# Optimization experiments

Hardware: AMD Instinct MI355X
Metric: run time of the kernel (lower is better)

Reference implementation:

```python
import jax, jax.numpy as jnp
import numpy as np

SIGMAS = (2.5, 4.0, 6.0, 9.0, 14.0)
TRUNCATE = 4.0
POOL = 16
COND_HIDDEN = 32


def _gauss_kernel_bank():
    """All K Gaussian kernels zero-padded (center-aligned) to a common length.
    Zero padding a centered symmetric kernel does not change the conv result,
    so a single grouped conv computes all K depthwise smoothings at once.
    Returns kernel bank [K, 1, L] and the common half-width pad."""
    ks = []
    for s in SIGMAS:
        r = max(1, int(TRUNCATE * s))
        xs = np.arange(-r, r + 1, dtype=np.float32)
        k = np.exp(-0.5 * (xs / s) ** 2)
        k = k / (k.sum() + 1e-12)
        ks.append(k)
    L = max(len(k) for k in ks)  # 113 for default sigmas
    bank = np.zeros((len(ks), 1, L), np.float32)
    for i, k in enumerate(ks):
        off = (L - len(k)) // 2
        bank[i, 0, off:off + len(k)] = k
    return jnp.asarray(bank), (L - 1) // 2


def setup_inputs() -> dict:
    key = jax.random.key(0)
    k0, k1, k2 = jax.random.split(key, 3)
    B, T, C = 16, 4096, 256
    H, K = COND_HIDDEN, len(SIGMAS)
    return {
        "x": jax.random.normal(k0, (B, T, C), jnp.float32),
        "W1": jax.random.normal(k1, (3, H), jnp.float32) * 0.5,
        "b1": jnp.zeros((H,), jnp.float32),
        "W2": jax.random.normal(k2, (H, K), jnp.float32) * 0.2,
        "b2": jnp.zeros((K,), jnp.float32),
    }


def reference(x, W1, b1, W2, b2):
    B, T, C = x.shape
    bank, pad = _gauss_kernel_bank()  # [K,1,L]
    # K depthwise Gaussian convs, fused into one grouped conv by treating
    # each (batch, channel) pair as an independent conv batch element.
    xin = x.transpose(0, 2, 1).reshape(B * C, 1, T)  # [B*C,1,T]
    y = jax.lax.conv_general_dilated(xin, bank, (1,), [(pad, pad)])  # [B*C,K,T]
    Y = y.reshape(B, C, -1, T).transpose(0, 3, 1, 2)  # [B,T,C,K]

    # local mean / variance with reflect padding (matches F.pad mode='reflect')
    pL = (POOL - 1) // 2
    pR = POOL - 1 - pL
    xp = jnp.pad(x, ((0, 0), (pL, pR), (0, 0)), mode="reflect")  # [B,T+POOL-1,C]
    cs = jnp.cumsum(xp, axis=1)
    cs = jnp.concatenate([jnp.zeros_like(cs[:, :1]), cs], axis=1)
    mean = (cs[:, POOL:] - cs[:, :-POOL]) / POOL  # [B,T,C]
    cs2 = jnp.cumsum(xp * xp, axis=1)
    cs2 = jnp.concatenate([jnp.zeros_like(cs2[:, :1]), cs2], axis=1)
    mean2 = (cs2[:, POOL:] - cs2[:, :-POOL]) / POOL
    var = jnp.maximum(mean2 - mean * mean, 0.0)

    # tiny per-position conditioner MLP -> softmax mixture weights over K
    feats = jnp.stack([mean, var, x], axis=-1)  # [B,T,C,3]
    h = jax.nn.gelu(feats @ W1 + b1, approximate=False)  # torch GELU = exact erf
    logits = h @ W2 + b2  # [B,T,C,K]
    w = jax.nn.softmax(logits, axis=-1)
    return (Y * w).sum(axis=-1)  # [B,T,C]
```

## Files before the change

### kernel.cpp

```cpp
#include <hip/hip_runtime.h>
#include <math.h>

#define T_LEN 4096
#define C_LEN 256
#define B_LEN 16

constexpr double cexp(double x) {
    double y = x * (1.0 / 1024.0);
    double t = 1.0, term = 1.0;
    for (int i = 1; i <= 12; ++i) { term *= y / i; t += term; }
    for (int i = 0; i < 10; ++i) t = t * t;
    return t;
}

constexpr int RAD[5] = {10, 16, 24, 36, 56};

struct Bank { float g[5][57]; };

constexpr Bank make_bank() {
    Bank b{};
    const double sig[5] = {2.5, 4.0, 6.0, 9.0, 14.0};
    for (int k = 0; k < 5; ++k) {
        double w[57] = {};
        for (int j = 0; j <= RAD[k]; ++j)
            w[j] = cexp(-0.5 * (double)(j * j) / (sig[k] * sig[k]));
        double s = w[0];
        for (int j = 1; j <= RAD[k]; ++j) s += 2.0 * w[j];
        s += 1e-12;
        for (int j = 0; j <= RAD[k]; ++j) b.g[k][j] = (float)(w[j] / s);
    }
    return b;
}

constexpr Bank BANK = make_bank();

#define LOG2E 1.4426950408889634f

__device__ __forceinline__ float fast_exp2(float x) {
#if __has_builtin(__builtin_amdgcn_exp2f)
    return __builtin_amdgcn_exp2f(x);
#else
    return __expf(x * 0.6931471805599453f);
#endif
}

__device__ __forceinline__ float gelu_fast(float v) {
    const float c1 = (float)(-2.0 * 0.7978845608028654 * 1.4426950408889634);
    const float c2 = c1 * 0.044715f;
    float v2 = v * v;
    float t  = fmaf(c2, v2, c1);
    float z  = v * t;
    float e  = fast_exp2(z);
    float r  = __builtin_amdgcn_rcpf(1.0f + e);
    return v * r;
}

__device__ __forceinline__ float ldz(const float* __restrict__ xb, int tt) {
    if (tt < 0 || tt >= T_LEN) return 0.0f;
    return xb[tt * C_LEN];
}

template <bool CHECKED>
__device__ __forceinline__ void work(const float* __restrict__ x,
                                     float* __restrict__ out,
                                     const float (*__restrict__ wle)[8],
                                     const float* __restrict__ w2e,
                                     const float* __restrict__ b2l,
                                     int b, int t0, int c) {
    const float* xb = x + (size_t)b * T_LEN * C_LEN + c;

    float v[19];
#pragma unroll
    for (int i = 0; i < 19; ++i) {
        int tt = t0 - 7 + i;
        if (CHECKED) {
            tt = (tt < 0) ? -tt : tt;
            tt = (tt >= T_LEN) ? (2 * T_LEN - 2 - tt) : tt;
        }
        v[i] = xb[tt * C_LEN];
    }

    float mean[4], var[4], xc[4];
    {
        float s = 0.f, q = 0.f;
#pragma unroll
        for (int i = 0; i < 16; ++i) { s += v[i]; q = fmaf(v[i], v[i], q); }
#pragma unroll
        for (int m = 0; m < 4; ++m) {
            if (m > 0) {
                float nw = v[15 + m], od = v[m - 1];
                s = s + nw - od;
                q = fmaf(nw, nw, fmaf(od, -od, q));
            }
            mean[m] = s * 0.0625f;
            float m2 = q * 0.0625f;
            float vv = fmaf(-mean[m], mean[m], m2);
            var[m] = vv > 0.f ? vv : 0.f;
            xc[m]  = v[7 + m];
        }
    }

    float acc[5][4];
#pragma unroll
    for (int k = 0; k < 5; ++k)
#pragma unroll
        for (int m = 0; m < 4; ++m) acc[k][m] = BANK.g[k][0] * xc[m];

    float F[4], Bw[4];
    if (CHECKED) {
        F[1] = ldz(xb, t0 + 1); F[2] = ldz(xb, t0 + 2);
        F[3] = ldz(xb, t0 + 3); F[0] = ldz(xb, t0 + 4);
        Bw[3] = ldz(xb, t0 - 1); Bw[0] = ldz(xb, t0);
        Bw[1] = ldz(xb, t0 + 1); Bw[2] = ldz(xb, t0 + 2);
    } else {
        F[1] = v[8]; F[2] = v[9]; F[3] = v[10]; F[0] = v[11];
        Bw[3] = v[6]; Bw[0] = v[7]; Bw[1] = v[8]; Bw[2] = v[9];
    }

#pragma unroll
    for (int j = 1; j <= 56; ++j) {
        float sm[4];
#pragma unroll
        for (int m = 0; m < 4; ++m)
            sm[m] = F[(j + m) & 3] + Bw[(m - j) & 3];
#pragma unroll
        for (int k = 0; k < 5; ++k) {
            if (j <= RAD[k]) {
#pragma unroll
                for (int m = 0; m < 4; ++m)
                    acc[k][m] = fmaf(BANK.g[k][j], sm[m], acc[k][m]);
            }
        }
        if (j < 56) {
            if (CHECKED) {
                F[j & 3]        = ldz(xb, t0 + j + 4);
                Bw[(3 - j) & 3] = ldz(xb, t0 - j - 1);
            } else {
                F[j & 3]        = (j <= 7) ? v[j + 11] : xb[(t0 + j + 4) * C_LEN];
                Bw[(3 - j) & 3] = (j <= 6) ? v[6 - j]  : xb[(t0 - j - 1) * C_LEN];
            }
        }
    }

    float lg[5][4];
#pragma unroll
    for (int k = 0; k < 5; ++k) {
        float bk = b2l[k];
#pragma unroll
        for (int m = 0; m < 4; ++m) lg[k][m] = bk;
    }

#pragma unroll 2
    for (int i = 0; i < 32; ++i) {
        float4 wa = *(const float4*)&wle[i][0];
        float4 wb = *(const float4*)&wle[i][4];
        float w24 = w2e[i];
#pragma unroll
        for (int m = 0; m < 4; ++m) {
            float pre = fmaf(wa.x, mean[m], fmaf(wa.y, var[m], fmaf(wa.z, xc[m], wa.w)));
            float h = gelu_fast(pre);
            lg[0][m] = fmaf(h, wb.x, lg[0][m]);
            lg[1][m] = fmaf(h, wb.y, lg[1][m]);
            lg[2][m] = fmaf(h, wb.z, lg[2][m]);
            lg[3][m] = fmaf(h, wb.w, lg[3][m]);
            lg[4][m] = fmaf(h, w24 , lg[4][m]);
        }
    }

#pragma unroll
    for (int m = 0; m < 4; ++m) {
        float l0 = lg[0][m], l1 = lg[1][m], l2 = lg[2][m], l3 = lg[3][m], l4 = lg[4][m];
        float mx = fmaxf(fmaxf(fmaxf(l0, l1), fmaxf(l2, l3)), l4);
        float e0 = fast_exp2(l0 - mx), e1 = fast_exp2(l1 - mx), e2 = fast_exp2(l2 - mx);
        float e3 = fast_exp2(l3 - mx), e4 = fast_exp2(l4 - mx);
        float den = ((e0 + e1) + (e2 + e3)) + e4;
        float num = e0 * acc[0][m];
        num = fmaf(e1, acc[1][m], num);
        num = fmaf(e2, acc[2][m], num);
        num = fmaf(e3, acc[3][m], num);
        num = fmaf(e4, acc[4][m], num);
        out[((size_t)b * T_LEN + t0 + m) * C_LEN + c] = num * __builtin_amdgcn_rcpf(den);
    }
}

__global__ __launch_bounds__(256) void agt_fused(
    const float* __restrict__ x, const float* __restrict__ W1,
    const float* __restrict__ b1, const float* __restrict__ W2,
    const float* __restrict__ b2, float* __restrict__ out) {
    __shared__ __align__(16) float wle[32][8];
    __shared__ float w2e[32];
    __shared__ float b2l[5];
    {
        int tid = threadIdx.x;
        if (tid < 32) {
            wle[tid][0] = W1[tid];
            wle[tid][1] = W1[32 + tid];
            wle[tid][2] = W1[64 + tid];
            wle[tid][3] = b1[tid];
            wle[tid][4] = W2[tid * 5 + 0] * LOG2E;
            wle[tid][5] = W2[tid * 5 + 1] * LOG2E;
            wle[tid][6] = W2[tid * 5 + 2] * LOG2E;
            wle[tid][7] = W2[tid * 5 + 3] * LOG2E;
            w2e[tid]    = W2[tid * 5 + 4] * LOG2E;
            if (tid < 5) b2l[tid] = b2[tid] * LOG2E;
        }
        __syncthreads();
    }
    int b     = blockIdx.x >> 10;
    int chunk = blockIdx.x & 1023;
    int t0    = chunk * 4;
    if (chunk >= 14 && chunk < 1010)
        work<false>(x, out, wle, w2e, b2l, b, t0, threadIdx.x);
    else
        work<true>(x, out, wle, w2e, b2l, b, t0, threadIdx.x);
}

extern "C" void kernel_launch(void* const* d_in, const int* in_sizes, int n_in,
                              void* d_out, int out_size, void* d_ws, size_t ws_size,
                              hipStream_t stream) {
    const float* x  = (const float*)d_in[0];
    const float* W1 = (const float*)d_in[1];
    const float* b1 = (const float*)d_in[2];
    const float* W2 = (const float*)d_in[3];
    const float* b2 = (const float*)d_in[4];
    float* out = (float*)d_out;

    (void)in_sizes; (void)n_in; (void)d_ws; (void)ws_size; (void)out_size;

    agt_fused<<<dim3(B_LEN * 1024), dim3(256), 0, stream>>>(x, W1, b1, W2, b2, out);
}
```

Before: 428.5 us.

## Run conditioner MLP on MFMA f16 matrix cores via per-wave LDS staging

Moves the per-position 3->32->5 conditioner MLP from scalar FMAs to MFMA 16x16x32 f16 instructions. Features (mean, var, x, 1) are packed to half precision in LDS, the hidden GELU activations are staged back through LDS as f16, and the logits are stored as f16 for the softmax. The goal is to cut the large VALU cost of the MLP, at the cost of f16 rounding of features, hidden values and logits. The softmax also drops the max subtraction, which risks overflow, and a min-blocks launch bound is added. Cross-lane LDS exchange relies only on compiler fences within a wave.

After: 1.263 ms. +194.7%, slower.

```diff
diff --git a/kernel.cpp b/kernel.cpp
--- a/kernel.cpp
+++ b/kernel.cpp
@@ -4,6 +4,8 @@
 #define T_LEN 4096
 #define C_LEN 256
 #define B_LEN 16
+#define LOG2E 1.4426950408889634f
+#define HSTR 80
 
 constexpr double cexp(double x) {
     double y = x * (1.0 / 1024.0);
@@ -34,7 +36,12 @@
 
 constexpr Bank BANK = make_bank();
 
-#define LOG2E 1.4426950408889634f
+typedef _Float16 hf;
+typedef hf    hfx2 __attribute__((ext_vector_type(2)));
+typedef hf    hfx8 __attribute__((ext_vector_type(8)));
+typedef float f32x4 __attribute__((ext_vector_type(4)));
+
+__device__ __forceinline__ void lds_fence() { asm volatile("" ::: "memory"); }
 
 __device__ __forceinline__ float fast_exp2(float x) {
 #if __has_builtin(__builtin_amdgcn_exp2f)
@@ -60,13 +67,38 @@
     return xb[tt * C_LEN];
 }
 
+struct Frags { hfx8 b1a, b1b, b2; f32x4 c2; };
+
+__device__ __forceinline__ Frags build_frags(const float* __restrict__ wraw, int lane) {
+    Frags f;
+    const int n = lane & 15, g = lane >> 4;
+    hfx8 z = {0, 0, 0, 0, 0, 0, 0, 0};
+    f.b1a = z; f.b1b = z;
+    if (g == 0) {
+        f.b1a[0] = (hf)wraw[n];      f.b1b[0] = (hf)wraw[16 + n];
+        f.b1a[1] = (hf)wraw[32 + n]; f.b1b[1] = (hf)wraw[48 + n];
+        f.b1a[2] = (hf)wraw[64 + n]; f.b1b[2] = (hf)wraw[80 + n];
+        f.b1a[3] = (hf)wraw[96 + n]; f.b1b[3] = (hf)wraw[112 + n];
+    }
+#pragma unroll
+    for (int j = 0; j < 8; ++j) {
+        int kk = 8 * g + j;
+        int canon = ((kk & 1) << 4) | (kk >> 1);
+        float wv = (n < 5) ? wraw[128 + canon * 5 + n] * LOG2E : 0.0f;
+        f.b2[j] = (hf)wv;
+    }
+    float cc = (n < 5) ? wraw[288 + n] * LOG2E : 0.0f;
+    f.c2 = (f32x4){cc, cc, cc, cc};
+    return f;
+}
+
 template <bool CHECKED>
 __device__ __forceinline__ void work(const float* __restrict__ x,
                                      float* __restrict__ out,
-                                     const float (*__restrict__ wle)[8],
-                                     const float* __restrict__ w2e,
-                                     const float* __restrict__ b2l,
-                                     int b, int t0, int c) {
+                                     const float* __restrict__ wraw,
+                                     char* __restrict__ fe,
+                                     char* __restrict__ hb,
+                                     int b, int t0, int c, int lane) {
     const float* xb = x + (size_t)b * T_LEN * C_LEN + c;
 
     float v[19];
@@ -100,6 +132,18 @@
         }
     }
 
+#pragma unroll
+    for (int m = 0; m < 4; ++m) {
+        auto p0 = __builtin_amdgcn_cvt_pkrtz(mean[m], var[m]);
+        auto p1 = __builtin_amdgcn_cvt_pkrtz(xc[m], 1.0f);
+        int4 r4;
+        r4.x = __builtin_bit_cast(int, p0);
+        r4.y = __builtin_bit_cast(int, p1);
+        r4.z = 0; r4.w = 0;
+        *(int4*)(fe + (m * 64 + lane) * 16) = r4;
+    }
+    lds_fence();
+
     float acc[5][4];
 #pragma unroll
     for (int k = 0; k < 5; ++k)
@@ -142,37 +186,47 @@
         }
     }
 
-    float lg[5][4];
-#pragma unroll
-    for (int k = 0; k < 5; ++k) {
-        float bk = b2l[k];
-#pragma unroll
-        for (int m = 0; m < 4; ++m) lg[k][m] = bk;
-    }
+    Frags fr = build_frags(wraw, lane);
+    const int rl = lane & 15, gq = lane >> 4;
+    const char* a1p = fe + rl * 16;
+    char*       hwp = hb + gq * (4 * HSTR) + rl * 4;
+    const char* a2p = hb + rl * HSTR + gq * 16;
+    char*       lwp = fe + gq * 64 + rl * 2;
+    const f32x4 z4 = (f32x4){0.f, 0.f, 0.f, 0.f};
 
 #pragma unroll 2
-    for (int i = 0; i < 32; ++i) {
-        float4 wa = *(const float4*)&wle[i][0];
-        float4 wb = *(const float4*)&wle[i][4];
-        float w24 = w2e[i];
-#pragma unroll
-        for (int m = 0; m < 4; ++m) {
-            float pre = fmaf(wa.x, mean[m], fmaf(wa.y, var[m], fmaf(wa.z, xc[m], wa.w)));
-            float h = gelu_fast(pre);
-            lg[0][m] = fmaf(h, wb.x, lg[0][m]);
-            lg[1][m] = fmaf(h, wb.y, lg[1][m]);
-            lg[2][m] = fmaf(h, wb.z, lg[2][m]);
-            lg[3][m] = fmaf(h, wb.w, lg[3][m]);
-            lg[4][m] = fmaf(h, w24 , lg[4][m]);
-        }
-    }
+    for (int t = 0; t < 16; ++t) {
+        hfx8 a1 = *(const hfx8*)(a1p + t * 256);
+        f32x4 d1a = __builtin_amdgcn_mfma_f32_16x16x32_f16(a1, fr.b1a, z4, 0, 0, 0);
+        f32x4 d1b = __builtin_amdgcn_mfma_f32_16x16x32_f16(a1, fr.b1b, z4, 0, 0, 0);
+#pragma unroll
+        for (int r = 0; r < 4; ++r) {
+            auto hp = __builtin_amdgcn_cvt_pkrtz(gelu_fast(d1a[r]), gelu_fast(d1b[r]));
+            *(int*)(hwp + r * HSTR) = __builtin_bit_cast(int, hp);
+        }
+        lds_fence();
+        hfx8 a2 = *(const hfx8*)a2p;
+        lds_fence();
+        f32x4 d2 = __builtin_amdgcn_mfma_f32_16x16x32_f16(a2, fr.b2, fr.c2, 0, 0, 0);
+        if (rl < 5) {
+#pragma unroll
+            for (int r = 0; r < 4; ++r)
+                *(hf*)(lwp + t * 256 + r * 16) = (hf)d2[r];
+        }
+    }
+    lds_fence();
 
 #pragma unroll
     for (int m = 0; m < 4; ++m) {
-        float l0 = lg[0][m], l1 = lg[1][m], l2 = lg[2][m], l3 = lg[3][m], l4 = lg[4][m];
-        float mx = fmaxf(fmaxf(fmaxf(l0, l1), fmaxf(l2, l3)), l4);
-        float e0 = fast_exp2(l0 - mx), e1 = fast_exp2(l1 - mx), e2 = fast_exp2(l2 - mx);
-        float e3 = fast_exp2(l3 - mx), e4 = fast_exp2(l4 - mx);
+        const char* Lr = fe + (m * 64 + lane) * 16;
+        hfx2 q01 = *(const hfx2*)(Lr);
+        hfx2 q23 = *(const hfx2*)(Lr + 4);
+        hf   q4  = *(const hf*)(Lr + 8);
+        float e0 = fast_exp2((float)q01[0]);
+        float e1 = fast_exp2((float)q01[1]);
+        float e2 = fast_exp2((float)q23[0]);
+        float e3 = fast_exp2((float)q23[1]);
+        float e4 = fast_exp2((float)q4);
         float den = ((e0 + e1) + (e2 + e3)) + e4;
         float num = e0 * acc[0][m];
         num = fmaf(e1, acc[1][m], num);
@@ -183,36 +237,36 @@
     }
 }
 
-__global__ __launch_bounds__(256) void agt_fused(
+__global__ __launch_bounds__(256, 4) void agt_fused(
     const float* __restrict__ x, const float* __restrict__ W1,
     const float* __restrict__ b1, const float* __restrict__ W2,
     const float* __restrict__ b2, float* __restrict__ out) {
-    __shared__ __align__(16) float wle[32][8];
-    __shared__ float w2e[32];
-    __shared__ float b2l[5];
-    {
-        int tid = threadIdx.x;
-        if (tid < 32) {
-            wle[tid][0] = W1[tid];
-            wle[tid][1] = W1[32 + tid];
-            wle[tid][2] = W1[64 + tid];
-            wle[tid][3] = b1[tid];
-            wle[tid][4] = W2[tid * 5 + 0] * LOG2E;
-            wle[tid][5] = W2[tid * 5 + 1] * LOG2E;
-            wle[tid][6] = W2[tid * 5 + 2] * LOG2E;
-            wle[tid][7] = W2[tid * 5 + 3] * LOG2E;
-            w2e[tid]    = W2[tid * 5 + 4] * LOG2E;
-            if (tid < 5) b2l[tid] = b2[tid] * LOG2E;
-        }
-        __syncthreads();
-    }
+    __shared__ float wraw[296];
+    __shared__ __align__(16) char fe_lds[4][4096];
+    __shared__ __align__(16) char h_lds[4][16 * HSTR];
+
+    int tid = threadIdx.x;
+    for (int i = tid; i < 293; i += 256) {
+        float w;
+        if (i < 96)       w = W1[i];
+        else if (i < 128) w = b1[i - 96];
+        else if (i < 288) w = W2[i - 128];
+        else              w = b2[i - 288];
+        wraw[i] = w;
+    }
+    __syncthreads();
+
     int b     = blockIdx.x >> 10;
     int chunk = blockIdx.x & 1023;
     int t0    = chunk * 4;
+    int lane  = tid & 63;
+    char* fe  = &fe_lds[tid >> 6][0];
+    char* hb  = &h_lds[tid >> 6][0];
+
     if (chunk >= 14 && chunk < 1010)
-        work<false>(x, out, wle, w2e, b2l, b, t0, threadIdx.x);
+        work<false>(x, out, wraw, fe, hb, b, t0, tid, lane);
     else
-        work<true>(x, out, wle, w2e, b2l, b, t0, threadIdx.x);
+        work<true>(x, out, wraw, fe, hb, b, t0, tid, lane);
 }
 
 extern "C" void kernel_launch(void* const* d_in, const int* in_sizes, int n_in,
```
